# Kernel tuning notes

Hardware: AMD Instinct MI355X
Metric: run time of the kernel (lower is better)

The kernel has to match this reference:

```python
import jax, jax.numpy as jnp
import numpy as np

N = 50000      # nodes
E = 400000     # edges (before self loops)
F_IN = 128     # num_features
HID = 64       # hidden_dim
HEADS = 4
G = 64         # number of graphs in batch
NCLS = 2
NEG = 0.2      # leaky relu negative slope
BN_EPS = 1e-5


def setup_inputs() -> dict:
    key = jax.random.key(0)
    ks = jax.random.split(key, 32)
    rn = lambda k, shape, s=0.05: jax.random.normal(k, shape, jnp.float32) * s
    inp = {}
    inp["x"] = jax.random.normal(ks[0], (N, F_IN), jnp.float32)
    inp["edge_index"] = jax.random.randint(ks[1], (2, E), 0, N, dtype=jnp.int32)
    inp["batch"] = jnp.sort(jax.random.randint(ks[2], (N,), 0, G, dtype=jnp.int32))
    # layer 0 GATConv (concat=True) + pre projection
    inp["conv0_W"] = rn(ks[3], (F_IN, HEADS * HID))
    inp["conv0_att_src"] = rn(ks[4], (HEADS, HID))
    inp["conv0_att_dst"] = rn(ks[5], (HEADS, HID))
    inp["conv0_bias"] = jnp.zeros((HEADS * HID,), jnp.float32)
    inp["pre0_W"] = rn(ks[6], (HEADS * HID, HID))
    inp["pre0_b"] = jnp.zeros((HID,), jnp.float32)
    # layers 1..2 GATConv (concat=False), stacked
    inp["convs_W"] = rn(ks[7], (2, HID, HEADS * HID))
    inp["convs_att_src"] = rn(ks[8], (2, HEADS, HID))
    inp["convs_att_dst"] = rn(ks[9], (2, HEADS, HID))
    inp["convs_bias"] = jnp.zeros((2, HID), jnp.float32)
    # batch norms (eval mode: running stats)
    inp["bn_gamma"] = jnp.ones((3, HID), jnp.float32)
    inp["bn_beta"] = jnp.zeros((3, HID), jnp.float32)
    inp["bn_mean"] = rn(ks[10], (3, HID), 0.1)
    inp["bn_var"] = jax.random.uniform(ks[11], (3, HID), jnp.float32) + 0.5
    # JK projection, attention pooling, classifier
    inp["jump_W"] = rn(ks[12], (3 * HID, HID))
    inp["jump_b"] = jnp.zeros((HID,), jnp.float32)
    inp["att_W"] = rn(ks[13], (HID, 1))
    inp["att_b"] = jnp.zeros((1,), jnp.float32)
    inp["cls_W1"] = rn(ks[14], (HID, HID // 2))
    inp["cls_b1"] = jnp.zeros((HID // 2,), jnp.float32)
    inp["cls_W2"] = rn(ks[15], (HID // 2, NCLS))
    inp["cls_b2"] = jnp.zeros((NCLS,), jnp.float32)
    return inp


def _segment_softmax(logits, seg, num_segments):
    m = jax.ops.segment_max(logits, seg, num_segments=num_segments)
    e = jnp.exp(logits - m[seg])
    s = jax.ops.segment_sum(e, seg, num_segments=num_segments)
    return e / s[seg]


def _gat_conv(x, src, dst, W, a_src, a_dst, bias, concat):
    n = x.shape[0]
    H, C = a_src.shape
    xh = (x @ W).reshape(n, H, C)                         # [N, H, C]
    as_n = jnp.einsum('nhc,hc->nh', xh, a_src)            # [N, H]
    ad_n = jnp.einsum('nhc,hc->nh', xh, a_dst)            # [N, H]
    logits = jax.nn.leaky_relu(as_n[src] + ad_n[dst], NEG)  # [E', H]
    att = _segment_softmax(logits, dst, n)                # softmax over incoming edges
    out = jax.ops.segment_sum(xh[src] * att[:, :, None], dst, num_segments=n)
    out = out.reshape(n, H * C) if concat else out.mean(axis=1)
    return out + bias


def _bn(h, g, b, m, v):
    return (h - m) * jax.lax.rsqrt(v + BN_EPS) * g + b


def reference(x, edge_index, batch, conv0_W, conv0_att_src, conv0_att_dst,
              conv0_bias, pre0_W, pre0_b, convs_W, convs_att_src, convs_att_dst,
              convs_bias, bn_gamma, bn_beta, bn_mean, bn_var, jump_W, jump_b,
              att_W, att_b, cls_W1, cls_b1, cls_W2, cls_b2):
    n = x.shape[0]
    loops = jnp.arange(n, dtype=edge_index.dtype)
    src = jnp.concatenate([edge_index[0], loops])         # add_self_loops=True
    dst = jnp.concatenate([edge_index[1], loops])
    reps = []
    # layer 0: concat heads -> pre projection -> BN -> ELU (no residual: 128 != 64)
    h = _gat_conv(x, src, dst, conv0_W, conv0_att_src, conv0_att_dst, conv0_bias, True)
    h = h @ pre0_W + pre0_b
    h = jax.nn.elu(_bn(h, bn_gamma[0], bn_beta[0], bn_mean[0], bn_var[0]))
    reps.append(h)
    # layers 1..2: mean heads -> BN -> ELU -> residual
    for i in range(2):
        h_in = h
        h = _gat_conv(h, src, dst, convs_W[i], convs_att_src[i], convs_att_dst[i],
                      convs_bias[i], False)
        h = jax.nn.elu(_bn(h, bn_gamma[i + 1], bn_beta[i + 1], bn_mean[i + 1], bn_var[i + 1]))
        h = h + h_in
        reps.append(h)
    # jumping knowledge (cat)
    h = jnp.concatenate(reps, axis=-1) @ jump_W + jump_b  # [N, HID]
    # attentional global pooling
    a = _segment_softmax((h @ att_W + att_b)[:, 0], batch, G)  # [N]
    hg = jax.ops.segment_sum(h * a[:, None], batch, num_segments=G)  # [G, HID]
    # classifier
    return jax.nn.relu(hg @ cls_W1 + cls_b1) @ cls_W2 + cls_b2
```

## Files before the change

### kernel.cpp

```cpp
#include <hip/hip_runtime.h>
#include <hip/hip_bf16.h>
#include <math.h>

#define NEG 0.2f
#define BNEPS 1e-5f
#define NGRAPH 64
#define SCAN_CHUNK 2048
#define POOL_BLOCKS 256

typedef short bf16x8 __attribute__((ext_vector_type(8)));
typedef float f32x4  __attribute__((ext_vector_type(4)));

__device__ __forceinline__ float bf2f(unsigned short u) {
    return __uint_as_float(((unsigned)u) << 16);
}
__device__ __forceinline__ short f2bf(float f) {
    return (short)__bfloat16_as_ushort(__float2bfloat16(f));
}

__global__ __launch_bounds__(256)
void gemm_xh_mfma(const float* __restrict__ A, int lda,
                  const float* __restrict__ W, int Nc, int M, int K,
                  const float* __restrict__ att_s, const float* __restrict__ att_d,
                  float* __restrict__ as_out, float* __restrict__ ad_out,
                  unsigned short* __restrict__ Cbf)
{
    __shared__ short Wt[64 * 136];
    const int KP = K + 8;
    int tid  = threadIdx.x;
    int lane = tid & 63, wave = tid >> 6;
    int row0 = blockIdx.x * 64;
    int colb = blockIdx.y * 64;
    int c15 = lane & 15, q = lane >> 4;

    {
        int n = tid & 63;
        for (int k = tid >> 6; k < K; k += 4)
            Wt[n * KP + k] = f2bf(W[(size_t)k * Nc + colb + n]);
    }
    __syncthreads();

    int row = row0 + wave * 16 + c15;
    bool rok = row < M;
    const float* arow = A + (size_t)row * lda + q * 8;

    f32x4 acc[4];
    #pragma unroll
    for (int st = 0; st < 4; ++st) acc[st] = (f32x4){0.f, 0.f, 0.f, 0.f};

    for (int k0 = 0; k0 < K; k0 += 32) {
        bf16x8 av;
        if (rok) {
            float4 a0 = *(const float4*)(arow + k0);
            float4 a1 = *(const float4*)(arow + k0 + 4);
            av[0] = f2bf(a0.x); av[1] = f2bf(a0.y); av[2] = f2bf(a0.z); av[3] = f2bf(a0.w);
            av[4] = f2bf(a1.x); av[5] = f2bf(a1.y); av[6] = f2bf(a1.z); av[7] = f2bf(a1.w);
        } else {
            av = (bf16x8){0,0,0,0,0,0,0,0};
        }
        #pragma unroll
        for (int st = 0; st < 4; ++st) {
            bf16x8 bv = *(const bf16x8*)(Wt + (st * 16 + c15) * KP + k0 + q * 8);
            acc[st] = __builtin_amdgcn_mfma_f32_16x16x32_bf16(av, bv, acc[st], 0, 0, 0);
        }
    }

    #pragma unroll
    for (int r = 0; r < 4; ++r) {
        int orow = row0 + wave * 16 + q * 4 + r;
        if (orow >= M) continue;
        unsigned short* cb = Cbf + (size_t)orow * 256 + colb + c15;
        #pragma unroll
        for (int st = 0; st < 4; ++st)
            cb[st * 16] = (unsigned short)f2bf(acc[st][r]);
    }
    float sa[4], da[4];
    #pragma unroll
    for (int st = 0; st < 4; ++st) {
        sa[st] = att_s[colb + st * 16 + c15];
        da[st] = att_d[colb + st * 16 + c15];
    }
    #pragma unroll
    for (int r = 0; r < 4; ++r) {
        float ps = acc[0][r] * sa[0] + acc[1][r] * sa[1] + acc[2][r] * sa[2] + acc[3][r] * sa[3];
        float pd = acc[0][r] * da[0] + acc[1][r] * da[1] + acc[2][r] * da[2] + acc[3][r] * da[3];
        #pragma unroll
        for (int o = 1; o < 16; o <<= 1) {
            ps += __shfl_xor(ps, o);
            pd += __shfl_xor(pd, o);
        }
        int orow = row0 + wave * 16 + q * 4 + r;
        if (c15 == 0 && orow < M) {
            as_out[orow * 4 + blockIdx.y] = ps;
            ad_out[orow * 4 + blockIdx.y] = pd;
        }
    }
}

__global__ __launch_bounds__(256)
void gemm_n64_mfma(const void* __restrict__ Araw, int lda, int a_is_bf16,
                   const float* __restrict__ W, int M, int K,
                   const float* __restrict__ bias,
                   float* __restrict__ C, int ldc, int mode,
                   const float* __restrict__ bn_g, const float* __restrict__ bn_b,
                   const float* __restrict__ bn_m, const float* __restrict__ bn_v,
                   const float* __restrict__ attW, const float* __restrict__ attb,
                   float* __restrict__ wout)
{
    __shared__ short Wt[64 * 264];
    const int KP = K + 8;
    int tid  = threadIdx.x;
    int lane = tid & 63, wave = tid >> 6;
    int row0 = blockIdx.x * 64;
    int c15 = lane & 15, q = lane >> 4;

    {
        int n = tid & 63;
        for (int k = tid >> 6; k < K; k += 4)
            Wt[n * KP + k] = f2bf(W[(size_t)k * 64 + n]);
    }
    __syncthreads();

    int row = row0 + wave * 16 + c15;
    bool rok = row < M;

    f32x4 acc[4];
    #pragma unroll
    for (int st = 0; st < 4; ++st) acc[st] = (f32x4){0.f, 0.f, 0.f, 0.f};

    for (int k0 = 0; k0 < K; k0 += 32) {
        bf16x8 av;
        if (rok) {
            if (a_is_bf16) {
                av = *(const bf16x8*)((const unsigned short*)Araw
                                      + (size_t)row * lda + k0 + q * 8);
            } else {
                const float* ap = (const float*)Araw + (size_t)row * lda + k0 + q * 8;
                float4 a0 = *(const float4*)ap;
                float4 a1 = *(const float4*)(ap + 4);
                av[0] = f2bf(a0.x); av[1] = f2bf(a0.y); av[2] = f2bf(a0.z); av[3] = f2bf(a0.w);
                av[4] = f2bf(a1.x); av[5] = f2bf(a1.y); av[6] = f2bf(a1.z); av[7] = f2bf(a1.w);
            }
        } else {
            av = (bf16x8){0,0,0,0,0,0,0,0};
        }
        #pragma unroll
        for (int st = 0; st < 4; ++st) {
            bf16x8 bv = *(const bf16x8*)(Wt + (st * 16 + c15) * KP + k0 + q * 8);
            acc[st] = __builtin_amdgcn_mfma_f32_16x16x32_bf16(av, bv, acc[st], 0, 0, 0);
        }
    }

    #pragma unroll
    for (int st = 0; st < 4; ++st) {
        int col = st * 16 + c15;
        float bs = bias ? bias[col] : 0.f;
        float sg = 1.f, sb = 0.f;
        if (mode == 1) {
            sg = bn_g[col] / sqrtf(bn_v[col] + BNEPS);
            sb = bn_b[col] - bn_m[col] * sg;
        }
        #pragma unroll
        for (int r = 0; r < 4; ++r) {
            int orow = row0 + wave * 16 + q * 4 + r;
            if (orow >= M) continue;
            float v = acc[st][r] + bs;
            if (mode == 1) {
                v = v * sg + sb;
                v = v > 0.f ? v : __expf(v) - 1.f;
            }
            acc[st][r] = v;
            C[(size_t)orow * ldc + col] = v;
        }
    }

    if (wout) {
        float sa[4];
        #pragma unroll
        for (int st = 0; st < 4; ++st) sa[st] = attW[st * 16 + c15];
        float ab = attb[0];
        #pragma unroll
        for (int r = 0; r < 4; ++r) {
            float ps = acc[0][r] * sa[0] + acc[1][r] * sa[1]
                     + acc[2][r] * sa[2] + acc[3][r] * sa[3];
            #pragma unroll
            for (int o = 1; o < 16; o <<= 1) ps += __shfl_xor(ps, o);
            int orow = row0 + wave * 16 + q * 4 + r;
            if (c15 == 0 && orow < M) wout[orow] = __expf(ps + ab);
        }
    }
}

__global__ __launch_bounds__(256)
void hist_kernel(const int* __restrict__ ei, int E, int N, int* __restrict__ counts)
{
    int e = blockIdx.x * blockDim.x + threadIdx.x;
    int Etot = E + N;
    if (e >= Etot) return;
    int d = (e < E) ? ei[E + e] : e - E;
    atomicAdd(&counts[d], 1);
}

__global__ __launch_bounds__(256)
void scan_phase1(const int* __restrict__ counts, int N, int* __restrict__ blocksum)
{
    __shared__ int wsum[4];
    int tid = threadIdx.x, lane = tid & 63, wave = tid >> 6;
    int base = blockIdx.x * SCAN_CHUNK;
    int s = 0;
    #pragma unroll
    for (int j = 0; j < SCAN_CHUNK / 256; ++j) {
        int idx = base + tid + j * 256;
        if (idx < N) s += counts[idx];
    }
    #pragma unroll
    for (int o = 32; o; o >>= 1) s += __shfl_xor(s, o);
    if (lane == 0) wsum[wave] = s;
    __syncthreads();
    if (tid == 0) blocksum[blockIdx.x] = wsum[0] + wsum[1] + wsum[2] + wsum[3];
}

__global__ void scan_phase2(const int* __restrict__ blocksum, int nb,
                            int* __restrict__ blockoff, int* __restrict__ rowptr, int N)
{
    int lane = threadIdx.x;
    int v = (lane < nb) ? blocksum[lane] : 0;
    int incl = v;
    #pragma unroll
    for (int o = 1; o < 64; o <<= 1) {
        int t = __shfl_up(incl, o);
        if (lane >= o) incl += t;
    }
    if (lane < nb) blockoff[lane + 1] = incl;
    if (lane == 0) blockoff[0] = 0;
    int total = __shfl(incl, nb - 1);
    if (lane == 0) rowptr[N] = total;
}

__global__ __launch_bounds__(256)
void scan_phase3(const int* __restrict__ counts, int N,
                 const int* __restrict__ blockoff,
                 int* __restrict__ rowptr, int* __restrict__ cursor)
{
    __shared__ int wsum[4];
    int tid = threadIdx.x, lane = tid & 63, wave = tid >> 6;
    int start = blockIdx.x * SCAN_CHUNK + tid * 8;
    int v[8];
    int s = 0;
    #pragma unroll
    for (int j = 0; j < 8; ++j) {
        v[j] = (start + j < N) ? counts[start + j] : 0;
        s += v[j];
    }
    int incl = s;
    #pragma unroll
    for (int o = 1; o < 64; o <<= 1) {
        int t = __shfl_up(incl, o);
        if (lane >= o) incl += t;
    }
    if (lane == 63) wsum[wave] = incl;
    __syncthreads();
    int woff = 0;
    #pragma unroll
    for (int w = 0; w < 4; ++w) if (w < wave) woff += wsum[w];
    int run = blockoff[blockIdx.x] + woff + incl - s;
    #pragma unroll
    for (int j = 0; j < 8; ++j) {
        int idx = start + j;
        if (idx < N) { rowptr[idx] = run; cursor[idx] = run; }
        run += v[j];
    }
}

__global__ __launch_bounds__(256)
void scatter_kernel(const int* __restrict__ ei, int E, int N,
                    int* __restrict__ cursor, int* __restrict__ csr_src)
{
    int e = blockIdx.x * blockDim.x + threadIdx.x;
    int Etot = E + N;
    if (e >= Etot) return;
    int s, d;
    if (e < E) { s = ei[e]; d = ei[E + e]; } else { s = d = e - E; }
    int pos = atomicAdd(&cursor[d], 1);
    csr_src[pos] = s;
}

__global__ __launch_bounds__(256)
void aggregate_kernel(const int* __restrict__ rowptr, const int* __restrict__ csr_src,
                      const float* __restrict__ as_n, const float* __restrict__ ad_n,
                      const unsigned short* __restrict__ xh,
                      const float* __restrict__ bias,
                      float* __restrict__ outp, int ldo,
                      int N, int mode,
                      const float* __restrict__ bn_g, const float* __restrict__ bn_b,
                      const float* __restrict__ bn_m, const float* __restrict__ bn_v,
                      const float* __restrict__ resid)
{
    int node = (blockIdx.x * blockDim.x + threadIdx.x) >> 6;
    int lane = threadIdx.x & 63;
    if (node >= N) return;
    int h = lane >> 4, li = lane & 15, grp = lane & 48;
    int e0 = rowptr[node], e1 = rowptr[node + 1];
    float adh = ad_n[node * 4 + h];

    float4 acc = make_float4(0.f, 0.f, 0.f, 0.f);
    float wsum = 0.f;

    for (int base = e0; base < e1; base += 16) {
        int cnt = e1 - base; if (cnt > 16) cnt = 16;
        int s = 0; float w = 0.f;
        if (li < cnt) {
            s = csr_src[base + li];
            float l = as_n[s * 4 + h] + adh;
            l = fmaxf(l, NEG * l);
            w = __expf(l);
        }
        int k = 0;
        for (; k + 3 < cnt; k += 4) {
            float w0 = __shfl(w, grp + k),     w1 = __shfl(w, grp + k + 1);
            float w2 = __shfl(w, grp + k + 2), w3 = __shfl(w, grp + k + 3);
            int s0 = __shfl(s, grp + k),       s1 = __shfl(s, grp + k + 1);
            int s2 = __shfl(s, grp + k + 2),   s3 = __shfl(s, grp + k + 3);
            ushort4 xv0 = *(const ushort4*)(xh + (size_t)s0 * 256 + lane * 4);
            ushort4 xv1 = *(const ushort4*)(xh + (size_t)s1 * 256 + lane * 4);
            ushort4 xv2 = *(const ushort4*)(xh + (size_t)s2 * 256 + lane * 4);
            ushort4 xv3 = *(const ushort4*)(xh + (size_t)s3 * 256 + lane * 4);
            acc.x += w0 * bf2f(xv0.x); acc.y += w0 * bf2f(xv0.y);
            acc.z += w0 * bf2f(xv0.z); acc.w += w0 * bf2f(xv0.w);
            acc.x += w1 * bf2f(xv1.x); acc.y += w1 * bf2f(xv1.y);
            acc.z += w1 * bf2f(xv1.z); acc.w += w1 * bf2f(xv1.w);
            acc.x += w2 * bf2f(xv2.x); acc.y += w2 * bf2f(xv2.y);
            acc.z += w2 * bf2f(xv2.z); acc.w += w2 * bf2f(xv2.w);
            acc.x += w3 * bf2f(xv3.x); acc.y += w3 * bf2f(xv3.y);
            acc.z += w3 * bf2f(xv3.z); acc.w += w3 * bf2f(xv3.w);
            wsum += (w0 + w1) + (w2 + w3);
        }
        for (; k < cnt; ++k) {
            float wk = __shfl(w, grp + k);
            int sk = __shfl(s, grp + k);
            ushort4 xv = *(const ushort4*)(xh + (size_t)sk * 256 + lane * 4);
            acc.x += wk * bf2f(xv.x); acc.y += wk * bf2f(xv.y);
            acc.z += wk * bf2f(xv.z); acc.w += wk * bf2f(xv.w);
            wsum += wk;
        }
    }

    float rw = 1.f / wsum;
    acc.x *= rw; acc.y *= rw; acc.z *= rw; acc.w *= rw;

    if (mode == 0) {
        float4 bs = *(const float4*)(bias + lane * 4);
        ushort4 pk;
        pk.x = (unsigned short)f2bf(acc.x + bs.x);
        pk.y = (unsigned short)f2bf(acc.y + bs.y);
        pk.z = (unsigned short)f2bf(acc.z + bs.z);
        pk.w = (unsigned short)f2bf(acc.w + bs.w);
        *(ushort4*)((unsigned short*)outp + (size_t)node * 256 + lane * 4) = pk;
    } else {
        #pragma unroll
        for (int off = 16; off <= 32; off <<= 1) {
            acc.x += __shfl_xor(acc.x, off);
            acc.y += __shfl_xor(acc.y, off);
            acc.z += __shfl_xor(acc.z, off);
            acc.w += __shfl_xor(acc.w, off);
        }
        if (lane < 16) {
            int cin = lane * 4;
            float4 bs = *(const float4*)(bias + cin);
            float4 g = *(const float4*)(bn_g + cin);
            float4 b = *(const float4*)(bn_b + cin);
            float4 m = *(const float4*)(bn_m + cin);
            float4 vv = *(const float4*)(bn_v + cin);
            float4 rs = *(const float4*)(resid + (size_t)node * ldo + cin);
            float o[4] = {acc.x, acc.y, acc.z, acc.w};
            float bb[4] = {bs.x, bs.y, bs.z, bs.w};
            float gg[4] = {g.x, g.y, g.z, g.w};
            float be[4] = {b.x, b.y, b.z, b.w};
            float mm[4] = {m.x, m.y, m.z, m.w};
            float va[4] = {vv.x, vv.y, vv.z, vv.w};
            float rr[4] = {rs.x, rs.y, rs.z, rs.w};
            float4 res;
            float* rp = &res.x;
            #pragma unroll
            for (int j = 0; j < 4; ++j) {
                float v = 0.25f * o[j] + bb[j];
                float sg = gg[j] / sqrtf(va[j] + BNEPS);
                v = (v - mm[j]) * sg + be[j];
                v = v > 0.f ? v : __expf(v) - 1.f;
                rp[j] = v + rr[j];
            }
            *(float4*)(outp + (size_t)node * ldo + cin) = res;
        }
    }
}

__global__ void gstart_kernel(const int* __restrict__ batch, int N, int* __restrict__ gstart,
                              float* __restrict__ hg_acc, float* __restrict__ wsum_acc)
{
    int t = threadIdx.x;
    for (int idx = t; idx < NGRAPH * 64; idx += 128) hg_acc[idx] = 0.f;
    if (t < NGRAPH) wsum_acc[t] = 0.f;
    if (t <= NGRAPH) {
        int lo = 0, hi = N;
        while (lo < hi) {
            int mid = (lo + hi) >> 1;
            if (batch[mid] < t) lo = mid + 1; else hi = mid;
        }
        gstart[t] = lo;
    }
}

__global__ __launch_bounds__(256)
void pool_partial(const float* __restrict__ hjk, const float* __restrict__ w,
                  const int* __restrict__ batch, const int* __restrict__ gstart,
                  float* __restrict__ hg_acc, float* __restrict__ wsum_acc, int N)
{
    __shared__ float red[256];
    __shared__ float wred[4];
    int tid = threadIdx.x;
    int c = tid & 63, q = tid >> 6;
    int slab = (N + POOL_BLOCKS - 1) / POOL_BLOCKS;
    int n0 = blockIdx.x * slab;
    int n1 = n0 + slab; if (n1 > N) n1 = N;
    if (n0 >= n1) return;
    int g0 = batch[n0], g1 = batch[n1 - 1];

    for (int g = g0; g <= g1; ++g) {
        int s = gstart[g];     if (s < n0) s = n0;
        int e = gstart[g + 1]; if (e > n1) e = n1;
        float acc = 0.f, ws = 0.f;
        for (int n = s + q; n < e; n += 4) {
            float wn = w[n];
            acc += wn * hjk[(size_t)n * 64 + c];
            if (c == 0) ws += wn;
        }
        red[tid] = acc;
        if (c == 0) wred[q] = ws;
        __syncthreads();
        if (q == 0) {
            float v = red[c] + red[64 + c] + red[128 + c] + red[192 + c];
            if (v != 0.f) atomicAdd(&hg_acc[g * 64 + c], v);
            if (c == 0) {
                float t = wred[0] + wred[1] + wred[2] + wred[3];
                if (t != 0.f) atomicAdd(&wsum_acc[g], t);
            }
        }
        __syncthreads();
    }
}

__global__ void cls_kernel(const float* __restrict__ hg_acc,
                           const float* __restrict__ wsum_acc,
                           const float* __restrict__ W1, const float* __restrict__ b1,
                           const float* __restrict__ W2, const float* __restrict__ b2,
                           float* __restrict__ out)
{
    int g = blockIdx.x, t = threadIdx.x;
    __shared__ float z[32];
    __shared__ float h[64];
    float wsum = wsum_acc[g];
    float rw = (wsum > 0.f) ? 1.f / wsum : 0.f;
    h[t] = hg_acc[g * 64 + t] * rw;
    h[t + 32] = hg_acc[g * 64 + t + 32] * rw;
    __syncthreads();
    float acc = b1[t];
    for (int k = 0; k < 64; ++k) acc += h[k] * W1[k * 32 + t];
    z[t] = fmaxf(acc, 0.f);
    __syncthreads();
    if (t < 2) {
        float o = b2[t];
        for (int j = 0; j < 32; ++j) o += z[j] * W2[j * 2 + t];
        out[g * 2 + t] = o;
    }
}

extern "C" void kernel_launch(void* const* d_in, const int* in_sizes, int n_in,
                              void* d_out, int out_size, void* d_ws, size_t ws_size,
                              hipStream_t stream)
{
    const float* x        = (const float*)d_in[0];
    const int*   ei       = (const int*)d_in[1];
    const int*   batch    = (const int*)d_in[2];
    const float* conv0_W  = (const float*)d_in[3];
    const float* conv0_as = (const float*)d_in[4];
    const float* conv0_ad = (const float*)d_in[5];
    const float* conv0_b  = (const float*)d_in[6];
    const float* pre0_W   = (const float*)d_in[7];
    const float* pre0_b   = (const float*)d_in[8];
    const float* convs_W  = (const float*)d_in[9];
    const float* convs_as = (const float*)d_in[10];
    const float* convs_ad = (const float*)d_in[11];
    const float* convs_b  = (const float*)d_in[12];
    const float* bn_g     = (const float*)d_in[13];
    const float* bn_b     = (const float*)d_in[14];
    const float* bn_m     = (const float*)d_in[15];
    const float* bn_v     = (const float*)d_in[16];
    const float* jump_W   = (const float*)d_in[17];
    const float* jump_b   = (const float*)d_in[18];
    const float* att_W    = (const float*)d_in[19];
    const float* att_b    = (const float*)d_in[20];
    const float* cls_W1   = (const float*)d_in[21];
    const float* cls_b1   = (const float*)d_in[22];
    const float* cls_W2   = (const float*)d_in[23];
    const float* cls_b2   = (const float*)d_in[24];
    float* out = (float*)d_out;

    const int N = in_sizes[0] / 128;
    const int E = in_sizes[1] / 2;
    const int Etot = E + N;
    const int nb = (N + SCAN_CHUNK - 1) / SCAN_CHUNK;

    float* ws      = (float*)d_ws;
    unsigned short* xh_bf   = (unsigned short*)ws;
    unsigned short* h256_bf = xh_bf + (size_t)N * 256;
    float* repsAll = (float*)(h256_bf + (size_t)N * 256);
    float* as_n    = repsAll + (size_t)N * 192;
    float* ad_n    = as_n + (size_t)N * 4;
    float* hjk     = ad_n + (size_t)N * 4;
    float* hg_acc  = hjk + (size_t)N * 64;
    float* wsum_acc= hg_acc + NGRAPH * 64;
    int*   rowptr  = (int*)(wsum_acc + NGRAPH);
    int*   cursor  = rowptr + (N + 1);
    int*   counts  = cursor + N;
    int*   csr_src = counts + N;
    int*   gstart  = csr_src + Etot;
    int*   blocksum = gstart + (NGRAPH + 1);
    int*   blockoff = blocksum + 64;
    float* wbuf    = as_n;

    dim3 blk(256);
    int node_wave_blocks = (N + 3) / 4;
    int edge_blocks      = (Etot + 255) / 256;

    hipMemsetAsync(counts, 0, (size_t)N * sizeof(int), stream);
    hist_kernel<<<edge_blocks, blk, 0, stream>>>(ei, E, N, counts);
    scan_phase1<<<nb, blk, 0, stream>>>(counts, N, blocksum);
    scan_phase2<<<1, 64, 0, stream>>>(blocksum, nb, blockoff, rowptr, N);
    scan_phase3<<<nb, blk, 0, stream>>>(counts, N, blockoff, rowptr, cursor);
    scatter_kernel<<<edge_blocks, blk, 0, stream>>>(ei, E, N, cursor, csr_src);

    {
        dim3 g1((N + 63) / 64, 4);
        gemm_xh_mfma<<<g1, blk, 0, stream>>>(x, 128, conv0_W, 256, N, 128,
                                             conv0_as, conv0_ad, as_n, ad_n, xh_bf);
        aggregate_kernel<<<node_wave_blocks, blk, 0, stream>>>(
            rowptr, csr_src, as_n, ad_n, xh_bf, conv0_b, (float*)h256_bf, 256, N, 0,
            nullptr, nullptr, nullptr, nullptr, nullptr);
        dim3 g2((N + 63) / 64, 1);
        gemm_n64_mfma<<<g2, blk, 0, stream>>>(h256_bf, 256, 1, pre0_W, N, 256,
                                              pre0_b, repsAll, 192, 1,
                                              bn_g, bn_b, bn_m, bn_v,
                                              nullptr, nullptr, nullptr);
    }

    for (int i = 0; i < 2; ++i) {
        dim3 g1((N + 63) / 64, 4);
        gemm_xh_mfma<<<g1, blk, 0, stream>>>(repsAll + i * 64, 192,
                                             convs_W + (size_t)i * 64 * 256, 256, N, 64,
                                             convs_as + i * 256, convs_ad + i * 256,
                                             as_n, ad_n, xh_bf);
        aggregate_kernel<<<node_wave_blocks, blk, 0, stream>>>(
            rowptr, csr_src, as_n, ad_n, xh_bf, convs_b + i * 64,
            repsAll + (i + 1) * 64, 192, N, 1,
            bn_g + (i + 1) * 64, bn_b + (i + 1) * 64,
            bn_m + (i + 1) * 64, bn_v + (i + 1) * 64,
            repsAll + i * 64);
    }

    {
        dim3 g2((N + 63) / 64, 1);
        gemm_n64_mfma<<<g2, blk, 0, stream>>>(repsAll, 192, 0, jump_W, N, 192,
                                              jump_b, hjk, 64, 0,
                                              nullptr, nullptr, nullptr, nullptr,
                                              att_W, att_b, wbuf);
    }

    gstart_kernel<<<1, 128, 0, stream>>>(batch, N, gstart, hg_acc, wsum_acc);
    pool_partial<<<POOL_BLOCKS, blk, 0, stream>>>(hjk, wbuf, batch, gstart,
                                                  hg_acc, wsum_acc, N);
    cls_kernel<<<NGRAPH, 32, 0, stream>>>(hg_acc, wsum_acc, cls_W1, cls_b1,
                                          cls_W2, cls_b2, out);
}
```

Baseline: 409.4 us.

## Compute all 256 output columns per block in feature-attention GEMM

The feature GEMM now gives each 64-row block all 256 output columns, with 16 accumulator tiles, instead of splitting columns across four blocks in a second grid dimension. The A rows are read and converted to bf16 once rather than four times. The weight matrix is staged through shared memory in K-chunks of 64. Attention logits for all four heads are written as one float4 per row. The cost is more registers per thread (64 accumulator floats), fewer blocks in flight, and a serial per-thread weight load loop with an extra barrier per chunk.

```diff
diff --git a/kernel.cpp b/kernel.cpp
--- a/kernel.cpp
+++ b/kernel.cpp
@@ -20,79 +20,95 @@
 
 __global__ __launch_bounds__(256)
 void gemm_xh_mfma(const float* __restrict__ A, int lda,
-                  const float* __restrict__ W, int Nc, int M, int K,
+                  const float* __restrict__ W, int M, int K,
                   const float* __restrict__ att_s, const float* __restrict__ att_d,
                   float* __restrict__ as_out, float* __restrict__ ad_out,
                   unsigned short* __restrict__ Cbf)
 {
-    __shared__ short Wt[64 * 136];
-    const int KP = K + 8;
+    __shared__ short Wt[256 * 72];
     int tid  = threadIdx.x;
     int lane = tid & 63, wave = tid >> 6;
     int row0 = blockIdx.x * 64;
-    int colb = blockIdx.y * 64;
     int c15 = lane & 15, q = lane >> 4;
-
-    {
-        int n = tid & 63;
-        for (int k = tid >> 6; k < K; k += 4)
-            Wt[n * KP + k] = f2bf(W[(size_t)k * Nc + colb + n]);
-    }
-    __syncthreads();
 
     int row = row0 + wave * 16 + c15;
     bool rok = row < M;
     const float* arow = A + (size_t)row * lda + q * 8;
 
-    f32x4 acc[4];
-    #pragma unroll
-    for (int st = 0; st < 4; ++st) acc[st] = (f32x4){0.f, 0.f, 0.f, 0.f};
-
-    for (int k0 = 0; k0 < K; k0 += 32) {
-        bf16x8 av;
-        if (rok) {
-            float4 a0 = *(const float4*)(arow + k0);
-            float4 a1 = *(const float4*)(arow + k0 + 4);
-            av[0] = f2bf(a0.x); av[1] = f2bf(a0.y); av[2] = f2bf(a0.z); av[3] = f2bf(a0.w);
-            av[4] = f2bf(a1.x); av[5] = f2bf(a1.y); av[6] = f2bf(a1.z); av[7] = f2bf(a1.w);
-        } else {
-            av = (bf16x8){0,0,0,0,0,0,0,0};
-        }
-        #pragma unroll
-        for (int st = 0; st < 4; ++st) {
-            bf16x8 bv = *(const bf16x8*)(Wt + (st * 16 + c15) * KP + k0 + q * 8);
-            acc[st] = __builtin_amdgcn_mfma_f32_16x16x32_bf16(av, bv, acc[st], 0, 0, 0);
-        }
+    f32x4 acc[16];
+    #pragma unroll
+    for (int st = 0; st < 16; ++st) acc[st] = (f32x4){0.f, 0.f, 0.f, 0.f};
+
+    for (int kh = 0; kh < K; kh += 64) {
+        {
+            int c = tid;
+            int kmax = K - kh; if (kmax > 64) kmax = 64;
+            for (int k = 0; k < kmax; ++k)
+                Wt[c * 72 + k] = f2bf(W[(size_t)(kh + k) * 256 + c]);
+        }
+        __syncthreads();
+
+        #pragma unroll
+        for (int k0 = 0; k0 < 64; k0 += 32) {
+            if (kh + k0 >= K) break;
+            bf16x8 av;
+            if (rok) {
+                const float* ap = arow + kh + k0;
+                float4 a0 = *(const float4*)ap;
+                float4 a1 = *(const float4*)(ap + 4);
+                av[0] = f2bf(a0.x); av[1] = f2bf(a0.y); av[2] = f2bf(a0.z); av[3] = f2bf(a0.w);
+                av[4] = f2bf(a1.x); av[5] = f2bf(a1.y); av[6] = f2bf(a1.z); av[7] = f2bf(a1.w);
+            } else {
+                av = (bf16x8){0,0,0,0,0,0,0,0};
+            }
+            #pragma unroll
+            for (int st = 0; st < 16; ++st) {
+                bf16x8 bv = *(const bf16x8*)(Wt + (st * 16 + c15) * 72 + k0 + q * 8);
+                acc[st] = __builtin_amdgcn_mfma_f32_16x16x32_bf16(av, bv, acc[st], 0, 0, 0);
+            }
+        }
+        __syncthreads();
     }
 
     #pragma unroll
     for (int r = 0; r < 4; ++r) {
         int orow = row0 + wave * 16 + q * 4 + r;
         if (orow >= M) continue;
-        unsigned short* cb = Cbf + (size_t)orow * 256 + colb + c15;
-        #pragma unroll
-        for (int st = 0; st < 4; ++st)
+        unsigned short* cb = Cbf + (size_t)orow * 256 + c15;
+        #pragma unroll
+        for (int st = 0; st < 16; ++st)
             cb[st * 16] = (unsigned short)f2bf(acc[st][r]);
     }
-    float sa[4], da[4];
-    #pragma unroll
-    for (int st = 0; st < 4; ++st) {
-        sa[st] = att_s[colb + st * 16 + c15];
-        da[st] = att_d[colb + st * 16 + c15];
+
+    float sa[16], da[16];
+    #pragma unroll
+    for (int st = 0; st < 16; ++st) {
+        sa[st] = att_s[st * 16 + c15];
+        da[st] = att_d[st * 16 + c15];
     }
     #pragma unroll
     for (int r = 0; r < 4; ++r) {
-        float ps = acc[0][r] * sa[0] + acc[1][r] * sa[1] + acc[2][r] * sa[2] + acc[3][r] * sa[3];
-        float pd = acc[0][r] * da[0] + acc[1][r] * da[1] + acc[2][r] * da[2] + acc[3][r] * da[3];
-        #pragma unroll
-        for (int o = 1; o < 16; o <<= 1) {
-            ps += __shfl_xor(ps, o);
-            pd += __shfl_xor(pd, o);
+        float ps[4], pd[4];
+        #pragma unroll
+        for (int h = 0; h < 4; ++h) {
+            float s = 0.f, d = 0.f;
+            #pragma unroll
+            for (int j = 0; j < 4; ++j) {
+                int st = h * 4 + j;
+                s += acc[st][r] * sa[st];
+                d += acc[st][r] * da[st];
+            }
+            #pragma unroll
+            for (int o = 1; o < 16; o <<= 1) {
+                s += __shfl_xor(s, o);
+                d += __shfl_xor(d, o);
+            }
+            ps[h] = s; pd[h] = d;
         }
         int orow = row0 + wave * 16 + q * 4 + r;
         if (c15 == 0 && orow < M) {
-            as_out[orow * 4 + blockIdx.y] = ps;
-            ad_out[orow * 4 + blockIdx.y] = pd;
+            *(float4*)(as_out + orow * 4) = make_float4(ps[0], ps[1], ps[2], ps[3]);
+            *(float4*)(ad_out + orow * 4) = make_float4(pd[0], pd[1], pd[2], pd[3]);
         }
     }
 }
@@ -531,6 +547,7 @@
     dim3 blk(256);
     int node_wave_blocks = (N + 3) / 4;
     int edge_blocks      = (Etot + 255) / 256;
+    int row_blocks       = (N + 63) / 64;
 
     hipMemsetAsync(counts, 0, (size_t)N * sizeof(int), stream);
     hist_kernel<<<edge_blocks, blk, 0, stream>>>(ei, E, N, counts);
@@ -540,25 +557,22 @@
     scatter_kernel<<<edge_blocks, blk, 0, stream>>>(ei, E, N, cursor, csr_src);
 
     {
-        dim3 g1((N + 63) / 64, 4);
-        gemm_xh_mfma<<<g1, blk, 0, stream>>>(x, 128, conv0_W, 256, N, 128,
-                                             conv0_as, conv0_ad, as_n, ad_n, xh_bf);
+        gemm_xh_mfma<<<row_blocks, blk, 0, stream>>>(x, 128, conv0_W, N, 128,
+                                                     conv0_as, conv0_ad, as_n, ad_n, xh_bf);
         aggregate_kernel<<<node_wave_blocks, blk, 0, stream>>>(
             rowptr, csr_src, as_n, ad_n, xh_bf, conv0_b, (float*)h256_bf, 256, N, 0,
             nullptr, nullptr, nullptr, nullptr, nullptr);
-        dim3 g2((N + 63) / 64, 1);
-        gemm_n64_mfma<<<g2, blk, 0, stream>>>(h256_bf, 256, 1, pre0_W, N, 256,
-                                              pre0_b, repsAll, 192, 1,
-                                              bn_g, bn_b, bn_m, bn_v,
-                                              nullptr, nullptr, nullptr);
+        gemm_n64_mfma<<<row_blocks, blk, 0, stream>>>(h256_bf, 256, 1, pre0_W, N, 256,
+                                                      pre0_b, repsAll, 192, 1,
+                                                      bn_g, bn_b, bn_m, bn_v,
+                                                      nullptr, nullptr, nullptr);
     }
 
     for (int i = 0; i < 2; ++i) {
-        dim3 g1((N + 63) / 64, 4);
-        gemm_xh_mfma<<<g1, blk, 0, stream>>>(repsAll + i * 64, 192,
-                                             convs_W + (size_t)i * 64 * 256, 256, N, 64,
-                                             convs_as + i * 256, convs_ad + i * 256,
-                                             as_n, ad_n, xh_bf);
+        gemm_xh_mfma<<<row_blocks, blk, 0, stream>>>(repsAll + i * 64, 192,
+                                                     convs_W + (size_t)i * 64 * 256, N, 64,
+                                                     convs_as + i * 256, convs_ad + i * 256,
+                                                     as_n, ad_n, xh_bf);
         aggregate_kernel<<<node_wave_blocks, blk, 0, stream>>>(
             rowptr, csr_src, as_n, ad_n, xh_bf, convs_b + i * 64,
             repsAll + (i + 1) * 64, 192, N, 1,
@@ -567,13 +581,10 @@
             repsAll + i * 64);
     }
 
-    {
-        dim3 g2((N + 63) / 64, 1);
-        gemm_n64_mfma<<<g2, blk, 0, stream>>>(repsAll, 192, 0, jump_W, N, 192,
-                                              jump_b, hjk, 64, 0,
-                                              nullptr, nullptr, nullptr, nullptr,
-                                              att_W, att_b, wbuf);
-    }
+    gemm_n64_mfma<<<row_blocks, blk, 0, stream>>>(repsAll, 192, 0, jump_W, N, 192,
+                                                  jump_b, hjk, 64, 0,
+                                                  nullptr, nullptr, nullptr, nullptr,
+                                                  att_W, att_b, wbuf);
 
     gstart_kernel<<<1, 128, 0, stream>>>(batch, N, gstart, hg_acc, wsum_acc);
     pool_partial<<<POOL_BLOCKS, blk, 0, stream>>>(hjk, wbuf, batch, gstart,
```

Result: no change. 415.8 us (+1.6%).

## Aggregate before projecting in GAT layers 1-2 and precompute attention projections

Applied to the files above, without the earlier changes.

For the two mean-head GAT layers, this folds W·att into small per-layer projection matrices, computed once by a tiny kernel. The attention logits can then come straight from the 64-wide input representation inside the preceding GEMM epilogue. Aggregation now gathers 64-wide bf16 rep rows per head instead of 256-wide projected rows, and a 256-to-64 GEMM with head-mean scaling, BN, ELU and residual runs afterwards. This removes the separate xh GEMM per layer and cuts gather bytes, but adds a K=256 GEMM and an extra bf16 write of reps.

```diff
diff --git a/kernel.cpp b/kernel.cpp
--- a/kernel.cpp
+++ b/kernel.cpp
@@ -99,13 +99,17 @@
 
 __global__ __launch_bounds__(256)
 void gemm_n64_mfma(const void* __restrict__ Araw, int lda, int a_is_bf16,
-                   const float* __restrict__ W, int M, int K,
+                   const float* __restrict__ W, int w_conv, int M, int K, float alpha,
                    const float* __restrict__ bias,
                    float* __restrict__ C, int ldc, int mode,
                    const float* __restrict__ bn_g, const float* __restrict__ bn_b,
                    const float* __restrict__ bn_m, const float* __restrict__ bn_v,
+                   const float* __restrict__ resid, int ldr,
                    const float* __restrict__ attW, const float* __restrict__ attb,
-                   float* __restrict__ wout)
+                   float* __restrict__ wout,
+                   const float* __restrict__ P,
+                   float* __restrict__ as_out, float* __restrict__ ad_out,
+                   unsigned short* __restrict__ Cbf)
 {
     __shared__ short Wt[64 * 264];
     const int KP = K + 8;
@@ -116,8 +120,11 @@
 
     {
         int n = tid & 63;
-        for (int k = tid >> 6; k < K; k += 4)
-            Wt[n * KP + k] = f2bf(W[(size_t)k * 64 + n]);
+        for (int k = tid >> 6; k < K; k += 4) {
+            float wv = w_conv ? W[(size_t)(k & 63) * 256 + (k >> 6) * 64 + n]
+                              : W[(size_t)k * 64 + n];
+            Wt[n * KP + k] = f2bf(wv);
+        }
     }
     __syncthreads();
 
@@ -164,13 +171,15 @@
         for (int r = 0; r < 4; ++r) {
             int orow = row0 + wave * 16 + q * 4 + r;
             if (orow >= M) continue;
-            float v = acc[st][r] + bs;
+            float v = alpha * acc[st][r] + bs;
             if (mode == 1) {
                 v = v * sg + sb;
                 v = v > 0.f ? v : __expf(v) - 1.f;
             }
+            if (resid) v += resid[(size_t)orow * ldr + col];
             acc[st][r] = v;
             C[(size_t)orow * ldc + col] = v;
+            if (Cbf) Cbf[(size_t)orow * 64 + col] = (unsigned short)f2bf(v);
         }
     }
 
@@ -189,6 +198,57 @@
             if (c15 == 0 && orow < M) wout[orow] = __expf(ps + ab);
         }
     }
+
+    if (P) {
+        float Ps[4][4], Pd[4][4];
+        #pragma unroll
+        for (int st = 0; st < 4; ++st) {
+            int col = st * 16 + c15;
+            #pragma unroll
+            for (int h = 0; h < 4; ++h) {
+                Ps[st][h] = P[col * 8 + h];
+                Pd[st][h] = P[col * 8 + 4 + h];
+            }
+        }
+        #pragma unroll
+        for (int r = 0; r < 4; ++r) {
+            float ps[4], pd[4];
+            #pragma unroll
+            for (int h = 0; h < 4; ++h) {
+                float s = acc[0][r] * Ps[0][h] + acc[1][r] * Ps[1][h]
+                        + acc[2][r] * Ps[2][h] + acc[3][r] * Ps[3][h];
+                float d = acc[0][r] * Pd[0][h] + acc[1][r] * Pd[1][h]
+                        + acc[2][r] * Pd[2][h] + acc[3][r] * Pd[3][h];
+                #pragma unroll
+                for (int o = 1; o < 16; o <<= 1) {
+                    s += __shfl_xor(s, o);
+                    d += __shfl_xor(d, o);
+                }
+                ps[h] = s; pd[h] = d;
+            }
+            int orow = row0 + wave * 16 + q * 4 + r;
+            if (c15 == 0 && orow < M) {
+                *(float4*)(as_out + orow * 4) = make_float4(ps[0], ps[1], ps[2], ps[3]);
+                *(float4*)(ad_out + orow * 4) = make_float4(pd[0], pd[1], pd[2], pd[3]);
+            }
+        }
+    }
+}
+
+__global__ void proj_kernel(const float* __restrict__ Wc,
+                            const float* __restrict__ att_s, const float* __restrict__ att_d,
+                            float* __restrict__ P)
+{
+    int t = threadIdx.x;
+    int r = t >> 2, h = t & 3;
+    float s = 0.f, d = 0.f;
+    for (int c = 0; c < 64; ++c) {
+        float w = Wc[r * 256 + h * 64 + c];
+        s += w * att_s[h * 64 + c];
+        d += w * att_d[h * 64 + c];
+    }
+    P[r * 8 + h] = s;
+    P[r * 8 + 4 + h] = d;
 }
 
 __global__ __launch_bounds__(256)
@@ -290,11 +350,7 @@
                       const float* __restrict__ as_n, const float* __restrict__ ad_n,
                       const unsigned short* __restrict__ xh,
                       const float* __restrict__ bias,
-                      float* __restrict__ outp, int ldo,
-                      int N, int mode,
-                      const float* __restrict__ bn_g, const float* __restrict__ bn_b,
-                      const float* __restrict__ bn_m, const float* __restrict__ bn_v,
-                      const float* __restrict__ resid)
+                      unsigned short* __restrict__ outbf, int N)
 {
     int node = (blockIdx.x * blockDim.x + threadIdx.x) >> 6;
     int lane = threadIdx.x & 63;
@@ -346,52 +402,77 @@
     }
 
     float rw = 1.f / wsum;
-    acc.x *= rw; acc.y *= rw; acc.z *= rw; acc.w *= rw;
-
-    if (mode == 0) {
-        float4 bs = *(const float4*)(bias + lane * 4);
-        ushort4 pk;
-        pk.x = (unsigned short)f2bf(acc.x + bs.x);
-        pk.y = (unsigned short)f2bf(acc.y + bs.y);
-        pk.z = (unsigned short)f2bf(acc.z + bs.z);
-        pk.w = (unsigned short)f2bf(acc.w + bs.w);
-        *(ushort4*)((unsigned short*)outp + (size_t)node * 256 + lane * 4) = pk;
-    } else {
-        #pragma unroll
-        for (int off = 16; off <= 32; off <<= 1) {
-            acc.x += __shfl_xor(acc.x, off);
-            acc.y += __shfl_xor(acc.y, off);
-            acc.z += __shfl_xor(acc.z, off);
-            acc.w += __shfl_xor(acc.w, off);
-        }
-        if (lane < 16) {
-            int cin = lane * 4;
-            float4 bs = *(const float4*)(bias + cin);
-            float4 g = *(const float4*)(bn_g + cin);
-            float4 b = *(const float4*)(bn_b + cin);
-            float4 m = *(const float4*)(bn_m + cin);
-            float4 vv = *(const float4*)(bn_v + cin);
-            float4 rs = *(const float4*)(resid + (size_t)node * ldo + cin);
-            float o[4] = {acc.x, acc.y, acc.z, acc.w};
-            float bb[4] = {bs.x, bs.y, bs.z, bs.w};
-            float gg[4] = {g.x, g.y, g.z, g.w};
-            float be[4] = {b.x, b.y, b.z, b.w};
-            float mm[4] = {m.x, m.y, m.z, m.w};
-            float va[4] = {vv.x, vv.y, vv.z, vv.w};
-            float rr[4] = {rs.x, rs.y, rs.z, rs.w};
-            float4 res;
-            float* rp = &res.x;
-            #pragma unroll
-            for (int j = 0; j < 4; ++j) {
-                float v = 0.25f * o[j] + bb[j];
-                float sg = gg[j] / sqrtf(va[j] + BNEPS);
-                v = (v - mm[j]) * sg + be[j];
-                v = v > 0.f ? v : __expf(v) - 1.f;
-                rp[j] = v + rr[j];
-            }
-            *(float4*)(outp + (size_t)node * ldo + cin) = res;
-        }
-    }
+    float4 bs = *(const float4*)(bias + lane * 4);
+    ushort4 pk;
+    pk.x = (unsigned short)f2bf(acc.x * rw + bs.x);
+    pk.y = (unsigned short)f2bf(acc.y * rw + bs.y);
+    pk.z = (unsigned short)f2bf(acc.z * rw + bs.z);
+    pk.w = (unsigned short)f2bf(acc.w * rw + bs.w);
+    *(ushort4*)(outbf + (size_t)node * 256 + lane * 4) = pk;
+}
+
+__global__ __launch_bounds__(256)
+void aggregate_rep_kernel(const int* __restrict__ rowptr, const int* __restrict__ csr_src,
+                          const float* __restrict__ as_n, const float* __restrict__ ad_n,
+                          const unsigned short* __restrict__ repbf,
+                          unsigned short* __restrict__ outbf, int N)
+{
+    int node = (blockIdx.x * blockDim.x + threadIdx.x) >> 6;
+    int lane = threadIdx.x & 63;
+    if (node >= N) return;
+    int h = lane >> 4, li = lane & 15, grp = lane & 48;
+    int e0 = rowptr[node], e1 = rowptr[node + 1];
+    float adh = ad_n[node * 4 + h];
+
+    float4 acc = make_float4(0.f, 0.f, 0.f, 0.f);
+    float wsum = 0.f;
+
+    for (int base = e0; base < e1; base += 16) {
+        int cnt = e1 - base; if (cnt > 16) cnt = 16;
+        int s = 0; float w = 0.f;
+        if (li < cnt) {
+            s = csr_src[base + li];
+            float l = as_n[s * 4 + h] + adh;
+            l = fmaxf(l, NEG * l);
+            w = __expf(l);
+        }
+        int k = 0;
+        for (; k + 3 < cnt; k += 4) {
+            float w0 = __shfl(w, grp + k),     w1 = __shfl(w, grp + k + 1);
+            float w2 = __shfl(w, grp + k + 2), w3 = __shfl(w, grp + k + 3);
+            int s0 = __shfl(s, grp + k),       s1 = __shfl(s, grp + k + 1);
+            int s2 = __shfl(s, grp + k + 2),   s3 = __shfl(s, grp + k + 3);
+            ushort4 xv0 = *(const ushort4*)(repbf + (size_t)s0 * 64 + li * 4);
+            ushort4 xv1 = *(const ushort4*)(repbf + (size_t)s1 * 64 + li * 4);
+            ushort4 xv2 = *(const ushort4*)(repbf + (size_t)s2 * 64 + li * 4);
+            ushort4 xv3 = *(const ushort4*)(repbf + (size_t)s3 * 64 + li * 4);
+            acc.x += w0 * bf2f(xv0.x); acc.y += w0 * bf2f(xv0.y);
+            acc.z += w0 * bf2f(xv0.z); acc.w += w0 * bf2f(xv0.w);
+            acc.x += w1 * bf2f(xv1.x); acc.y += w1 * bf2f(xv1.y);
+            acc.z += w1 * bf2f(xv1.z); acc.w += w1 * bf2f(xv1.w);
+            acc.x += w2 * bf2f(xv2.x); acc.y += w2 * bf2f(xv2.y);
+            acc.z += w2 * bf2f(xv2.z); acc.w += w2 * bf2f(xv2.w);
+            acc.x += w3 * bf2f(xv3.x); acc.y += w3 * bf2f(xv3.y);
+            acc.z += w3 * bf2f(xv3.z); acc.w += w3 * bf2f(xv3.w);
+            wsum += (w0 + w1) + (w2 + w3);
+        }
+        for (; k < cnt; ++k) {
+            float wk = __shfl(w, grp + k);
+            int sk = __shfl(s, grp + k);
+            ushort4 xv = *(const ushort4*)(repbf + (size_t)sk * 64 + li * 4);
+            acc.x += wk * bf2f(xv.x); acc.y += wk * bf2f(xv.y);
+            acc.z += wk * bf2f(xv.z); acc.w += wk * bf2f(xv.w);
+            wsum += wk;
+        }
+    }
+
+    float rw = 1.f / wsum;
+    ushort4 pk;
+    pk.x = (unsigned short)f2bf(acc.x * rw);
+    pk.y = (unsigned short)f2bf(acc.y * rw);
+    pk.z = (unsigned short)f2bf(acc.z * rw);
+    pk.w = (unsigned short)f2bf(acc.w * rw);
+    *(ushort4*)(outbf + (size_t)node * 256 + lane * 4) = pk;
 }
 
 __global__ void gstart_kernel(const int* __restrict__ batch, int N, int* __restrict__ gstart,
@@ -513,11 +594,14 @@
     float* ws      = (float*)d_ws;
     unsigned short* xh_bf   = (unsigned short*)ws;
     unsigned short* h256_bf = xh_bf + (size_t)N * 256;
-    float* repsAll = (float*)(h256_bf + (size_t)N * 256);
+    unsigned short* repbf   = h256_bf + (size_t)N * 256;
+    float* repsAll = (float*)(repbf + (size_t)N * 64);
     float* as_n    = repsAll + (size_t)N * 192;
     float* ad_n    = as_n + (size_t)N * 4;
     float* hjk     = ad_n + (size_t)N * 4;
-    float* hg_acc  = hjk + (size_t)N * 64;
+    float* P1      = hjk + (size_t)N * 64;
+    float* P2      = P1 + 512;
+    float* hg_acc  = P2 + 512;
     float* wsum_acc= hg_acc + NGRAPH * 64;
     int*   rowptr  = (int*)(wsum_acc + NGRAPH);
     int*   cursor  = rowptr + (N + 1);
@@ -531,6 +615,7 @@
     dim3 blk(256);
     int node_wave_blocks = (N + 3) / 4;
     int edge_blocks      = (Etot + 255) / 256;
+    int row_blocks       = (N + 63) / 64;
 
     hipMemsetAsync(counts, 0, (size_t)N * sizeof(int), stream);
     hist_kernel<<<edge_blocks, blk, 0, stream>>>(ei, E, N, counts);
@@ -538,42 +623,43 @@
     scan_phase2<<<1, 64, 0, stream>>>(blocksum, nb, blockoff, rowptr, N);
     scan_phase3<<<nb, blk, 0, stream>>>(counts, N, blockoff, rowptr, cursor);
     scatter_kernel<<<edge_blocks, blk, 0, stream>>>(ei, E, N, cursor, csr_src);
+    proj_kernel<<<1, 256, 0, stream>>>(convs_W, convs_as, convs_ad, P1);
+    proj_kernel<<<1, 256, 0, stream>>>(convs_W + 64 * 256, convs_as + 256,
+                                       convs_ad + 256, P2);
 
     {
-        dim3 g1((N + 63) / 64, 4);
+        dim3 g1(row_blocks, 4);
         gemm_xh_mfma<<<g1, blk, 0, stream>>>(x, 128, conv0_W, 256, N, 128,
                                              conv0_as, conv0_ad, as_n, ad_n, xh_bf);
         aggregate_kernel<<<node_wave_blocks, blk, 0, stream>>>(
-            rowptr, csr_src, as_n, ad_n, xh_bf, conv0_b, (float*)h256_bf, 256, N, 0,
-            nullptr, nullptr, nullptr, nullptr, nullptr);
-        dim3 g2((N + 63) / 64, 1);
-        gemm_n64_mfma<<<g2, blk, 0, stream>>>(h256_bf, 256, 1, pre0_W, N, 256,
-                                              pre0_b, repsAll, 192, 1,
-                                              bn_g, bn_b, bn_m, bn_v,
-                                              nullptr, nullptr, nullptr);
+            rowptr, csr_src, as_n, ad_n, xh_bf, conv0_b, h256_bf, N);
+        gemm_n64_mfma<<<row_blocks, blk, 0, stream>>>(
+            h256_bf, 256, 1, pre0_W, 0, N, 256, 1.f, pre0_b,
+            repsAll, 192, 1, bn_g, bn_b, bn_m, bn_v,
+            nullptr, 0, nullptr, nullptr, nullptr,
+            P1, as_n, ad_n, repbf);
     }
 
     for (int i = 0; i < 2; ++i) {
-        dim3 g1((N + 63) / 64, 4);
-        gemm_xh_mfma<<<g1, blk, 0, stream>>>(repsAll + i * 64, 192,
-                                             convs_W + (size_t)i * 64 * 256, 256, N, 64,
-                                             convs_as + i * 256, convs_ad + i * 256,
-                                             as_n, ad_n, xh_bf);
-        aggregate_kernel<<<node_wave_blocks, blk, 0, stream>>>(
-            rowptr, csr_src, as_n, ad_n, xh_bf, convs_b + i * 64,
-            repsAll + (i + 1) * 64, 192, N, 1,
+        aggregate_rep_kernel<<<node_wave_blocks, blk, 0, stream>>>(
+            rowptr, csr_src, as_n, ad_n, repbf, xh_bf, N);
+        gemm_n64_mfma<<<row_blocks, blk, 0, stream>>>(
+            xh_bf, 256, 1, convs_W + (size_t)i * 64 * 256, 1, N, 256, 0.25f,
+            convs_b + i * 64,
+            repsAll + (i + 1) * 64, 192, 1,
             bn_g + (i + 1) * 64, bn_b + (i + 1) * 64,
             bn_m + (i + 1) * 64, bn_v + (i + 1) * 64,
-            repsAll + i * 64);
-    }
-
-    {
-        dim3 g2((N + 63) / 64, 1);
-        gemm_n64_mfma<<<g2, blk, 0, stream>>>(repsAll, 192, 0, jump_W, N, 192,
-                                              jump_b, hjk, 64, 0,
-                                              nullptr, nullptr, nullptr, nullptr,
-                                              att_W, att_b, wbuf);
-    }
+            repsAll + i * 64, 192,
+            nullptr, nullptr, nullptr,
+            (i == 0) ? P2 : nullptr, as_n, ad_n,
+            (i == 0) ? repbf : nullptr);
+    }
+
+    gemm_n64_mfma<<<row_blocks, blk, 0, stream>>>(
+        repsAll, 192, 0, jump_W, 0, N, 192, 1.f, jump_b,
+        hjk, 64, 0, nullptr, nullptr, nullptr, nullptr,
+        nullptr, 0, att_W, att_b, wbuf,
+        nullptr, nullptr, nullptr, nullptr);
 
     gstart_kernel<<<1, 128, 0, stream>>>(batch, N, gstart, hg_acc, wsum_acc);
     pool_partial<<<POOL_BLOCKS, blk, 0, stream>>>(hjk, wbuf, batch, gstart,
```

After: 419.1 us. +2.4%, slower.
